# Kernel optimization log

Hardware: AMD Instinct MI355X
Metric: run time of the kernel (lower is better)

## Reference

```python
import jax, jax.numpy as jnp
import numpy as np

N_NODES = 20000
N_EDGES = 320000
DIM = 256
OUT_DIM = 256
N_LAYERS = 2
AVG_LOG = float(np.log(17.0))  # PNA avg_deg['log'] from deg histogram (all degree 16)
STD_EPS = 1e-5
N_AGG = 5
N_SCALER = 3


def _pna_conv(x, edge_index, Wpre, bpre, Wpost, bpost, Wlin, blin):
    """PyG PNAConv (towers=1, pre_layers=1, post_layers=1, divide_input=False)."""
    N = x.shape[0]
    src, dst = edge_index[0], edge_index[1]  # messages flow src -> dst
    # pre_nn on concat([x_i, x_j]) per edge: [E, 2F] -> [E, F]
    m = jnp.concatenate([x[dst], x[src]], axis=-1) @ Wpre.T + bpre
    deg = jax.ops.segment_sum(jnp.ones((src.shape[0],), x.dtype), dst, num_segments=N)
    degc = jnp.maximum(deg, 1.0)[:, None]
    s = jax.ops.segment_sum(m, dst, num_segments=N)
    mean = s / degc
    mean2 = jax.ops.segment_sum(m * m, dst, num_segments=N) / degc
    std = jnp.sqrt(jax.nn.relu(mean2 - mean * mean) + STD_EPS)
    has = (deg > 0)[:, None]
    mn = jnp.where(has, jax.ops.segment_min(m, dst, num_segments=N), 0.0)
    mx = jnp.where(has, jax.ops.segment_max(m, dst, num_segments=N), 0.0)
    agg = jnp.concatenate([mean, s, std, mn, mx], axis=-1)  # [N, 5F]
    logd = jnp.log(degc + 1.0)
    scaled = jnp.concatenate(
        [agg, agg * (logd / AVG_LOG), agg * (AVG_LOG / logd)], axis=-1)  # [N, 15F]
    h = jnp.concatenate([x, scaled], axis=-1) @ Wpost.T + bpost  # [N, F_out]
    return h @ Wlin.T + blin


def setup_inputs() -> dict:
    key = jax.random.key(0)
    ks = jax.random.split(key, 20)
    F = DIM
    L = N_LAYERS
    post_in = (N_AGG * N_SCALER + 1) * F  # 16F = 4096
    sc = 0.05
    inp = {
        "x": jax.random.normal(ks[0], (N_NODES, F), jnp.float32),
        "edge_index_in": jax.random.randint(ks[1], (2, N_EDGES), 0, N_NODES),
        "edge_index_out": jax.random.randint(ks[2], (2, N_EDGES), 0, N_NODES),
    }
    def p(k, shape):
        return sc * jax.random.normal(k, shape, jnp.float32)
    # stacked per-layer params; supply (_s) and demand (_d) channels
    for tag, base in (("s", 3), ("d", 9)):
        inp[f"Wpre_{tag}"] = p(ks[base + 0], (L, F, 2 * F))
        inp[f"bpre_{tag}"] = p(ks[base + 1], (L, F))
        inp[f"Wpost_{tag}"] = p(ks[base + 2], (L, OUT_DIM, post_in))
        inp[f"bpost_{tag}"] = p(ks[base + 3], (L, OUT_DIM))
        inp[f"Wlin_{tag}"] = p(ks[base + 4], (L, OUT_DIM, OUT_DIM))
        inp[f"blin_{tag}"] = p(ks[base + 5], (L, OUT_DIM))
    inp["Wcomb"] = p(ks[15], (L, OUT_DIM, F + 2 * OUT_DIM))
    inp["bcomb"] = p(ks[16], (L, OUT_DIM))
    inp["Wout"] = p(ks[17], (1, OUT_DIM))
    inp["bout"] = p(ks[18], (1,))
    return inp


def reference(x, edge_index_in, edge_index_out,
              Wpre_s, bpre_s, Wpost_s, bpost_s, Wlin_s, blin_s,
              Wpre_d, bpre_d, Wpost_d, bpost_d, Wlin_d, blin_d,
              Wcomb, bcomb, Wout, bout):
    for l in range(N_LAYERS):
        h_in = jax.nn.relu(_pna_conv(x, edge_index_in,
                                     Wpre_s[l], bpre_s[l], Wpost_s[l], bpost_s[l],
                                     Wlin_s[l], blin_s[l]))
        h_out = jax.nn.relu(_pna_conv(x, edge_index_out,
                                      Wpre_d[l], bpre_d[l], Wpost_d[l], bpost_d[l],
                                      Wlin_d[l], blin_d[l]))
        x = jax.nn.relu(jnp.concatenate([x, h_in, h_out], axis=-1) @ Wcomb[l].T + bcomb[l])
    return jnp.squeeze(x @ Wout.T + bout)  # [N]
```

## Files before the change

### kernel.cpp

```cpp
#include <hip/hip_runtime.h>
#include <math.h>

#define NN 20000
#define NE 320000
#define AVG_LOG_F 2.83321334f

typedef unsigned short u16;
typedef _Float16 h8_t __attribute__((ext_vector_type(8)));
typedef float f4_t __attribute__((ext_vector_type(4)));

__device__ __forceinline__ u16 f2h(float f) {
  _Float16 h = (_Float16)f;
  return __builtin_bit_cast(u16, h);
}
__device__ __forceinline__ void gld16(const void* g, void* l) {
  __builtin_amdgcn_global_load_lds(
      (const __attribute__((address_space(1))) void*)g,
      (__attribute__((address_space(3))) void*)l, 16, 0, 0);
}

__global__ __launch_bounds__(256) void k_count2(const int* __restrict__ ein,
                                                const int* __restrict__ eout,
                                                int* __restrict__ deg2, int E) {
  int e = blockIdx.x * 256 + threadIdx.x;
  int ch = blockIdx.y;
  const int* dst = (ch ? eout : ein) + E;
  if (e < E) atomicAdd(&deg2[ch * NN + dst[e]], 1);
}

__global__ __launch_bounds__(1024) void k_scan(const int* __restrict__ deg,
                                               int* __restrict__ rp, int N) {
  __shared__ int lds[1024];
  int t = threadIdx.x;
  int CH = (N + 1023) >> 10;
  int base = t * CH;
  int s = 0;
  for (int i = 0; i < CH; ++i) { int idx = base + i; if (idx < N) s += deg[idx]; }
  lds[t] = s;
  __syncthreads();
  for (int off = 1; off < 1024; off <<= 1) {
    int v = (t >= off) ? lds[t - off] : 0;
    __syncthreads();
    lds[t] += v;
    __syncthreads();
  }
  int run = (t == 0) ? 0 : lds[t - 1];
  for (int i = 0; i < CH; ++i) {
    int idx = base + i;
    if (idx < N) { rp[idx] = run; run += deg[idx]; }
  }
  if (t == 1023) rp[N] = run;
}

__global__ __launch_bounds__(256) void k_scatter2(const int* __restrict__ ein,
                                                  const int* __restrict__ eout,
                                                  const int* __restrict__ rp2,
                                                  int* __restrict__ cur2,
                                                  int* __restrict__ col2, int E) {
  int e = blockIdx.x * 256 + threadIdx.x;
  int ch = blockIdx.y;
  const int* src = (ch ? eout : ein);
  const int* dst = src + E;
  if (e < E) {
    int d = dst[e];
    int p = atomicAdd(&cur2[ch * NN + d], 1);
    col2[rp2[ch * NN + d] + p] = src[e];
  }
}

__global__ __launch_bounds__(256) void k_cvtw(
    const float* __restrict__ Wpre_s, const float* __restrict__ Wpre_d,
    const float* __restrict__ Wlin_s, const float* __restrict__ Wlin_d,
    const float* __restrict__ Wcomb,
    u16* __restrict__ preS, u16* __restrict__ preD,
    u16* __restrict__ lincat, u16* __restrict__ combB) {
  int i = blockIdx.x * 256 + threadIdx.x;
  const float* src;
  u16* dst;
  int so, dofs;
  if (i < 65536)       { src = Wpre_s; dst = preS;  so = i;          dofs = so; }
  else if (i < 131072) { src = Wpre_d; dst = preD;  so = i - 65536;  dofs = so; }
  else if (i < 163840) { int j = i - 131072; int lyr = j >> 14;
                         src = Wlin_s; dst = lincat; so = j; dofs = j + lyr * 16384; }
  else if (i < 196608) { int j = i - 163840; int lyr = j >> 14;
                         src = Wlin_d; dst = lincat; so = j; dofs = j + (lyr + 1) * 16384; }
  else if (i < 294912) { src = Wcomb; dst = combB; so = i - 196608; dofs = so; }
  else return;
  float4 v = *(const float4*)(src + (size_t)so * 4);
  ushort4 o;
  o.x = f2h(v.x); o.y = f2h(v.y); o.z = f2h(v.z); o.w = f2h(v.w);
  *(ushort4*)(dst + (size_t)dofs * 4) = o;
}

__global__ __launch_bounds__(256) void k_cvtx(const float* __restrict__ x,
                                              u16* __restrict__ xc) {
  int i = blockIdx.x * 256 + threadIdx.x;
  int row = i >> 6, c = (i & 63) * 4;
  float4 v = *(const float4*)(x + (size_t)row * 256 + c);
  ushort4 o;
  o.x = f2h(v.x); o.y = f2h(v.y); o.z = f2h(v.z); o.w = f2h(v.w);
  *(ushort4*)(xc + (size_t)row * 768 + c) = o;
}

__global__ __launch_bounds__(256) void k_tc4(const float* __restrict__ Ws,
                                             const float* __restrict__ Wd,
                                             u16* __restrict__ outT) {
  __shared__ float tile[32][33];
  int z = blockIdx.z;
  const float* in = ((z & 1) ? Wd : Ws) + (size_t)(z >> 1) * 256 * 4096;
  u16* out = outT + (size_t)z * (4096 * 256);
  int bx = blockIdx.x, by = blockIdx.y;
  int r = threadIdx.x >> 5, c = threadIdx.x & 31;
#pragma unroll
  for (int it = 0; it < 4; ++it)
    tile[r + it * 8][c] = in[(size_t)(by * 32 + r + it * 8) * 4096 + bx * 32 + c];
  __syncthreads();
#pragma unroll
  for (int it = 0; it < 4; ++it)
    out[(size_t)(bx * 32 + r + it * 8) * 256 + by * 32 + c] = f2h(tile[c][r + it * 8]);
}

__global__ __launch_bounds__(512) void k_mgemm(
    const u16* __restrict__ A, int lda,
    const u16* __restrict__ B, const u16* __restrict__ B2, int ldb, int nsplit,
    const float* __restrict__ bias,
    u16* __restrict__ oH, int ldoH,
    int M, int K, int relu, int zA, int zB, int zO) {
  __shared__ u16 As[2][64 * 64];
  __shared__ u16 Bs[2][256 * 64];
  const int t = threadIdx.x;
  const int z = blockIdx.z;
  A += (size_t)z * zA;
  B += (size_t)z * zB;
  B2 += (size_t)z * zB;
  oH += (size_t)z * zO;
  const int m0 = blockIdx.y * 64;
  const int n0 = blockIdx.x * 256;
  const int l = t & 63, w = t >> 6;
  const int wm = w >> 2, wn = w & 3;
  const int lo = l & 15, hi = l >> 4;

  f4_t acc[2][4];
#pragma unroll
  for (int i = 0; i < 2; ++i)
#pragma unroll
    for (int j = 0; j < 4; ++j) acc[i][j] = (f4_t)0.f;

  const int ra = t >> 3, pa = t & 7;
  const int la = pa ^ (ra & 7);
  int rra = m0 + ra;
  if (rra > M - 1) rra = M - 1;
  const u16* gA = A + (size_t)rra * lda + la * 8;

  const u16* gB[4];
  int lBo[4];
#pragma unroll
  for (int i = 0; i < 4; ++i) {
    int q = i * 512 + t;
    int r = q >> 3, p2 = q & 7;
    int lc = p2 ^ (r & 7);
    int n = n0 + r;
    const u16* bp = (n < nsplit) ? (B + (size_t)n * ldb) : (B2 + (size_t)(n - nsplit) * ldb);
    gB[i] = bp + lc * 8;
    lBo[i] = q * 8;
  }

  gld16(gA, &As[0][t * 8]);
#pragma unroll
  for (int i = 0; i < 4; ++i) gld16(gB[i], &Bs[0][lBo[i]]);
  __syncthreads();

  const int nt = K >> 6;
  for (int tt = 0; tt < nt; ++tt) {
    const int cur = tt & 1;
    if (tt + 1 < nt) {
      const int ko = (tt + 1) << 6;
      gld16(gA + ko, &As[cur ^ 1][t * 8]);
#pragma unroll
      for (int i = 0; i < 4; ++i) gld16(gB[i] + ko, &Bs[cur ^ 1][lBo[i]]);
    }
#pragma unroll
    for (int ks = 0; ks < 2; ++ks) {
      h8_t af[2], bfr[4];
#pragma unroll
      for (int mi = 0; mi < 2; ++mi) {
        int row = wm * 32 + mi * 16 + lo;
        int c = (ks * 4 + hi) ^ (row & 7);
        af[mi] = *(const h8_t*)&As[cur][row * 64 + c * 8];
      }
#pragma unroll
      for (int ni = 0; ni < 4; ++ni) {
        int row = wn * 64 + ni * 16 + lo;
        int c = (ks * 4 + hi) ^ (row & 7);
        bfr[ni] = *(const h8_t*)&Bs[cur][row * 64 + c * 8];
      }
#pragma unroll
      for (int mi = 0; mi < 2; ++mi)
#pragma unroll
        for (int ni = 0; ni < 4; ++ni)
          acc[mi][ni] = __builtin_amdgcn_mfma_f32_16x16x32_f16(
              af[mi], bfr[ni], acc[mi][ni], 0, 0, 0);
    }
    __syncthreads();
  }

  float bv[4];
#pragma unroll
  for (int ni = 0; ni < 4; ++ni) {
    int n = n0 + wn * 64 + ni * 16 + lo;
    bv[ni] = (n < nsplit) ? (bias ? bias[n] : 0.f) : 0.f;
  }
#pragma unroll
  for (int mi = 0; mi < 2; ++mi) {
#pragma unroll
    for (int r = 0; r < 4; ++r) {
      int m = m0 + wm * 32 + mi * 16 + hi * 4 + r;
      if (m < M) {
#pragma unroll
        for (int ni = 0; ni < 4; ++ni) {
          int n = n0 + wn * 64 + ni * 16 + lo;
          float v = acc[mi][ni][r] + bv[ni];
          if (relu && v < 0.f) v = 0.f;
          oH[(size_t)m * ldoH + n] = f2h(v);
        }
      }
    }
  }
}

__global__ __launch_bounds__(512) void k_pgemm(
    const u16* __restrict__ xc, const u16* __restrict__ agg5c,
    const float* __restrict__ scal3c, const u16* __restrict__ Wfl,
    const float* __restrict__ bfl, u16* __restrict__ oHb, int M) {
  __shared__ u16 As[2][64 * 64];
  __shared__ u16 Bs[2][256 * 64];
  const int t = threadIdx.x;
  const int ch = blockIdx.y;
  const u16* agg5 = agg5c + (size_t)ch * NN * 1280;
  const float* scal3 = scal3c + (size_t)ch * NN * 4;
  const u16* Wf = Wfl + (size_t)ch * (256 * 4096);
  const float* bf = bfl + ch * 256;
  u16* oH = oHb + 256 + ch * 256;
  const int m0 = blockIdx.x * 64;
  const int l = t & 63, w = t >> 6;
  const int wm = w >> 2, wn = w & 3;
  const int lo = l & 15, hi = l >> 4;

  f4_t acc[2][4];
#pragma unroll
  for (int i = 0; i < 2; ++i)
#pragma unroll
    for (int j = 0; j < 4; ++j) acc[i][j] = (f4_t)0.f;

  const int ra = t >> 3, pa = t & 7;
  int m = m0 + ra;
  if (m > M - 1) m = M - 1;
  const u16* xrow = xc + (size_t)m * 768;
  const u16* arow = agg5 + (size_t)m * 1280;
  const float s1 = scal3[(size_t)m * 4 + 1];
  const float s2 = scal3[(size_t)m * 4 + 2];
  const int aslot = ra * 64 + (pa ^ (ra & 7)) * 8;

  const u16* gB[4];
  int lBo[4];
#pragma unroll
  for (int i = 0; i < 4; ++i) {
    int q = i * 512 + t;
    int r = q >> 3, p2 = q & 7;
    int lc = p2 ^ (r & 7);
    gB[i] = Wf + (size_t)r * 4096 + lc * 8;
    lBo[i] = q * 8;
  }

  {
    h8_t va = *(const h8_t*)(xrow + pa * 8);
#pragma unroll
    for (int i = 0; i < 4; ++i) gld16(gB[i], &Bs[0][lBo[i]]);
    *(h8_t*)&As[0][aslot] = va;
  }
  __syncthreads();

  for (int tt = 0; tt < 64; ++tt) {
    const int cur = tt & 1;
    h8_t va2 = (h8_t)(_Float16)0.f;
    float fac = 1.f;
    if (tt < 63) {
      int k = ((tt + 1) << 6) + pa * 8;
      const u16* ap;
      if (k < 256) {
        ap = xrow + k;
      } else {
        int q = k - 256;
        int r2 = q < 1280 ? q : (q < 2560 ? q - 1280 : q - 2560);
        fac = q < 1280 ? 1.f : (q < 2560 ? s1 : s2);
        ap = arow + r2;
      }
      va2 = *(const h8_t*)ap;
#pragma unroll
      for (int i = 0; i < 4; ++i) gld16(gB[i] + ((tt + 1) << 6), &Bs[cur ^ 1][lBo[i]]);
    }
#pragma unroll
    for (int ks = 0; ks < 2; ++ks) {
      h8_t af[2], bfr[4];
#pragma unroll
      for (int mi = 0; mi < 2; ++mi) {
        int row = wm * 32 + mi * 16 + lo;
        int c = (ks * 4 + hi) ^ (row & 7);
        af[mi] = *(const h8_t*)&As[cur][row * 64 + c * 8];
      }
#pragma unroll
      for (int ni = 0; ni < 4; ++ni) {
        int row = wn * 64 + ni * 16 + lo;
        int c = (ks * 4 + hi) ^ (row & 7);
        bfr[ni] = *(const h8_t*)&Bs[cur][row * 64 + c * 8];
      }
#pragma unroll
      for (int mi = 0; mi < 2; ++mi)
#pragma unroll
        for (int ni = 0; ni < 4; ++ni)
          acc[mi][ni] = __builtin_amdgcn_mfma_f32_16x16x32_f16(
              af[mi], bfr[ni], acc[mi][ni], 0, 0, 0);
    }
    if (tt < 63) *(h8_t*)&As[cur ^ 1][aslot] = va2 * (_Float16)fac;
    __syncthreads();
  }

  float bv[4];
#pragma unroll
  for (int ni = 0; ni < 4; ++ni) bv[ni] = bf[wn * 64 + ni * 16 + lo];
#pragma unroll
  for (int mi = 0; mi < 2; ++mi) {
#pragma unroll
    for (int r = 0; r < 4; ++r) {
      int mr = m0 + wm * 32 + mi * 16 + hi * 4 + r;
      if (mr < M) {
#pragma unroll
        for (int ni = 0; ni < 4; ++ni) {
          int n = wn * 64 + ni * 16 + lo;
          float vv = acc[mi][ni][r] + bv[ni];
          if (vv < 0.f) vv = 0.f;
          oH[(size_t)mr * 768 + n] = f2h(vv);
        }
      }
    }
  }
}

__global__ __launch_bounds__(256) void k_aggregate(
    const u16* __restrict__ AB, const int* __restrict__ rp,
    const int* __restrict__ col, u16* __restrict__ agg5,
    float* __restrict__ scal3) {
  int w = threadIdx.x >> 6, l = threadIdx.x & 63;
  int n = blockIdx.x * 4 + w;
  int beg = rp[n], end = rp[n + 1];
  int deg = end - beg;
  int half = l >> 5, lf = l & 31;
  float sb[8], qb[8], mnb[8], mxb[8];
#pragma unroll
  for (int j = 0; j < 8; ++j) {
    sb[j] = 0.f; qb[j] = 0.f;
    mnb[j] = 3.402823466e38f; mxb[j] = -3.402823466e38f;
  }
  for (int i = beg + half; i < end; i += 2) {
    int s = col[i];
    h8_t bv = *(const h8_t*)(AB + (size_t)s * 512 + 256 + lf * 8);
#pragma unroll
    for (int j = 0; j < 8; ++j) {
      float b = (float)bv[j];
      sb[j] += b;
      qb[j] = fmaf(b, b, qb[j]);
      mnb[j] = fminf(mnb[j], b);
      mxb[j] = fmaxf(mxb[j], b);
    }
  }
#pragma unroll
  for (int j = 0; j < 8; ++j) {
    sb[j] += __shfl_xor(sb[j], 32, 64);
    qb[j] += __shfl_xor(qb[j], 32, 64);
    mnb[j] = fminf(mnb[j], __shfl_xor(mnb[j], 32, 64));
    mxb[j] = fmaxf(mxb[j], __shfl_xor(mxb[j], 32, 64));
  }
  h8_t cv = *(const h8_t*)(AB + (size_t)n * 512 + lf * 8);
  float degf = (float)deg;
  float degc = degf > 1.f ? degf : 1.f;
  float inv = 1.f / degc;
  float ov[5][8];
#pragma unroll
  for (int j = 0; j < 8; ++j) {
    float c = (float)cv[j];
    float s_m = fmaf(degf, c, sb[j]);
    float mean = s_m * inv;
    float mean2 = fmaf(degf * c, c, fmaf(2.f * c, sb[j], qb[j])) * inv;
    float var = mean2 - mean * mean;
    if (var < 0.f) var = 0.f;
    float sd = sqrtf(var + 1e-5f);
    ov[0][j] = mean;
    ov[1][j] = s_m;
    ov[2][j] = sd;
    ov[3][j] = deg > 0 ? c + mnb[j] : 0.f;
    ov[4][j] = deg > 0 ? c + mxb[j] : 0.f;
  }
  if (half == 0) {
    u16* base = agg5 + (size_t)n * 1280 + lf * 8;
#pragma unroll
    for (int a = 0; a < 5; ++a) {
      h8_t o;
#pragma unroll
      for (int j = 0; j < 8; ++j) o[j] = (_Float16)ov[a][j];
      *(h8_t*)(base + a * 256) = o;
    }
    if (lf == 0) {
      float logd = logf(degc + 1.f);
      float4 sc = make_float4(1.f, logd / AVG_LOG_F, AVG_LOG_F / logd, 0.f);
      *(float4*)(scal3 + (size_t)n * 4) = sc;
    }
  }
}

__global__ __launch_bounds__(256) void k_bfuse4(
    const float* __restrict__ Wlin_s, const float* __restrict__ Wlin_d,
    const float* __restrict__ bpost_s, const float* __restrict__ bpost_d,
    const float* __restrict__ blin_s, const float* __restrict__ blin_d,
    float* __restrict__ bfv4) {
  __shared__ float bp[256];
  int z = blockIdx.x, lyr = z >> 1, ch = z & 1;
  const float* Wlin = (ch ? Wlin_d : Wlin_s) + (size_t)lyr * 65536;
  const float* bpost = (ch ? bpost_d : bpost_s) + lyr * 256;
  const float* blin = (ch ? blin_d : blin_s) + lyr * 256;
  int t = threadIdx.x;
  bp[t] = bpost[t];
  __syncthreads();
  float s = blin[t];
  for (int k = 0; k < 256; ++k) s = fmaf(Wlin[t * 256 + k], bp[k], s);
  bfv4[z * 256 + t] = s;
}

__global__ __launch_bounds__(256) void k_wout(const u16* __restrict__ x,
                                              const float* __restrict__ w,
                                              const float* __restrict__ b,
                                              float* __restrict__ out, int N) {
  int wid = threadIdx.x >> 6, lane = threadIdx.x & 63;
  int n = blockIdx.x * 4 + wid;
  if (n >= N) return;
  ushort4 xv = *(const ushort4*)(x + (size_t)n * 256 + lane * 4);
  const float4 wv = *(const float4*)(w + lane * 4);
  float s = (float)__builtin_bit_cast(_Float16, xv.x) * wv.x +
            (float)__builtin_bit_cast(_Float16, xv.y) * wv.y +
            (float)__builtin_bit_cast(_Float16, xv.z) * wv.z +
            (float)__builtin_bit_cast(_Float16, xv.w) * wv.w;
#pragma unroll
  for (int off = 32; off > 0; off >>= 1) s += __shfl_down(s, off);
  if (lane == 0) out[n] = s + b[0];
}

extern "C" void kernel_launch(void* const* d_in, const int* in_sizes, int n_in,
                              void* d_out, int out_size, void* d_ws, size_t ws_size,
                              hipStream_t stream) {
  const float* x0      = (const float*)d_in[0];
  const int*   ei_in   = (const int*)d_in[1];
  const int*   ei_out  = (const int*)d_in[2];
  const float* Wpre_s  = (const float*)d_in[3];
  const float* bpre_s  = (const float*)d_in[4];
  const float* Wpost_s = (const float*)d_in[5];
  const float* bpost_s = (const float*)d_in[6];
  const float* Wlin_s  = (const float*)d_in[7];
  const float* blin_s  = (const float*)d_in[8];
  const float* Wpre_d  = (const float*)d_in[9];
  const float* bpre_d  = (const float*)d_in[10];
  const float* Wpost_d = (const float*)d_in[11];
  const float* bpost_d = (const float*)d_in[12];
  const float* Wlin_d  = (const float*)d_in[13];
  const float* blin_d  = (const float*)d_in[14];
  const float* Wcomb   = (const float*)d_in[15];
  const float* bcomb   = (const float*)d_in[16];
  const float* Wout    = (const float*)d_in[17];
  const float* bout    = (const float*)d_in[18];
  float* out = (float*)d_out;

  char* p = (char*)d_ws;
  auto alloc = [&](size_t b) {
    char* r = p;
    p += (b + 255) & ~(size_t)255;
    return r;
  };
  int* deg2     = (int*)alloc((size_t)2 * NN * 4);
  int* cur2     = (int*)alloc((size_t)2 * NN * 4);
  int* rp2      = (int*)alloc((size_t)(2 * NN + 1) * 4);
  int* col2     = (int*)alloc((size_t)2 * NE * 4);
  u16* AB       = (u16*)alloc((size_t)NN * 512 * 2);
  u16* agg52    = (u16*)alloc((size_t)2 * NN * 1280 * 2);
  float* scal32 = (float*)alloc((size_t)2 * NN * 4 * 4);
  u16* xcat1    = (u16*)alloc((size_t)NN * 768 * 2);
  u16* xcat2    = (u16*)alloc((size_t)NN * 768 * 2);
  u16* preS     = (u16*)alloc((size_t)2 * 256 * 512 * 2);
  u16* preD     = (u16*)alloc((size_t)2 * 256 * 512 * 2);
  u16* lincat   = (u16*)alloc((size_t)4 * 256 * 256 * 2);
  u16* combB    = (u16*)alloc((size_t)2 * 256 * 768 * 2);
  u16* Wf4      = (u16*)alloc((size_t)4 * 256 * 4096 * 2);
  float* bfv4   = (float*)alloc((size_t)4 * 256 * 4);
  u16* WpostT4  = (u16*)agg52;
  u16* xfin     = xcat1;

  const int BIG = 1 << 30;

  k_cvtw<<<1152, 256, 0, stream>>>(Wpre_s, Wpre_d, Wlin_s, Wlin_d, Wcomb,
                                   preS, preD, lincat, combB);
  k_cvtx<<<5000, 256, 0, stream>>>(x0, xcat1);
  hipMemsetAsync(deg2, 0, (size_t)4 * NN * 4, stream);
  k_count2<<<dim3(1250, 2), 256, 0, stream>>>(ei_in, ei_out, deg2, NE);
  k_scan<<<1, 1024, 0, stream>>>(deg2, rp2, 2 * NN);
  k_scatter2<<<dim3(1250, 2), 256, 0, stream>>>(ei_in, ei_out, rp2, cur2, col2, NE);
  k_tc4<<<dim3(128, 8, 4), 256, 0, stream>>>(Wpost_s, Wpost_d, WpostT4);
  k_mgemm<<<dim3(16, 4, 4), 512, 0, stream>>>(
      lincat, 256, WpostT4, WpostT4, 256, BIG, nullptr,
      Wf4, 4096, 256, 256, 0, 65536, 1048576, 1048576);
  k_bfuse4<<<4, 256, 0, stream>>>(Wlin_s, Wlin_d, bpost_s, bpost_d, blin_s, blin_d, bfv4);

  u16* xcs[2] = {xcat1, xcat2};
  for (int lyr = 0; lyr < 2; ++lyr) {
    u16* xc = xcs[lyr];
    for (int ch = 0; ch < 2; ++ch) {
      u16* preW = ch ? preD : preS;
      const float* bpre = ch ? bpre_d : bpre_s;
      k_mgemm<<<dim3(2, 313, 1), 512, 0, stream>>>(
          xc, 768, preW + (size_t)lyr * 131072, preW + (size_t)lyr * 131072 + 256,
          512, 256, bpre + (size_t)lyr * 256,
          AB, 512, NN, 256, 0, 0, 0, 0);
      k_aggregate<<<5000, 256, 0, stream>>>(
          AB, rp2 + ch * NN, col2,
          agg52 + (size_t)ch * NN * 1280, scal32 + (size_t)ch * NN * 4);
    }
    k_pgemm<<<dim3(313, 2), 512, 0, stream>>>(
        xc, agg52, scal32, Wf4 + (size_t)lyr * 2 * 1048576, bfv4 + lyr * 512, xc, NN);
    if (lyr == 0) {
      k_mgemm<<<dim3(1, 313, 1), 512, 0, stream>>>(
          xc, 768, combB, combB, 768, BIG, bcomb,
          xcat2, 768, NN, 768, 1, 0, 0, 0);
    } else {
      k_mgemm<<<dim3(1, 313, 1), 512, 0, stream>>>(
          xc, 768, combB + 196608, combB + 196608, 768, BIG, bcomb + 256,
          xfin, 256, NN, 768, 1, 0, 0, 0);
    }
  }
  k_wout<<<5000, 256, 0, stream>>>(xfin, Wout, bout, out, NN);
}
```

Baseline: 852.4 us.

## Batch both channels' pre-GEMM and aggregation, single-buffer pgemm LDS

The pre-message GEMM and the aggregation for the supply and demand channels now each run as a single launch over a z/y grid dimension. This uses interleaved pre weights, a per-z bias and a doubled AB buffer, halving launches per layer and giving each kernel more blocks. Separately, k_pgemm's double-buffered LDS pipeline is replaced by a single buffer with load-then-sync per K step. That halves LDS use to allow more resident blocks, but loses the overlap of global loads with MFMA work.

```diff
diff --git a/kernel.cpp b/kernel.cpp
--- a/kernel.cpp
+++ b/kernel.cpp
@@ -72,14 +72,17 @@
     const float* __restrict__ Wpre_s, const float* __restrict__ Wpre_d,
     const float* __restrict__ Wlin_s, const float* __restrict__ Wlin_d,
     const float* __restrict__ Wcomb,
-    u16* __restrict__ preS, u16* __restrict__ preD,
-    u16* __restrict__ lincat, u16* __restrict__ combB) {
+    u16* __restrict__ pre2, u16* __restrict__ lincat, u16* __restrict__ combB) {
   int i = blockIdx.x * 256 + threadIdx.x;
   const float* src;
   u16* dst;
   int so, dofs;
-  if (i < 65536)       { src = Wpre_s; dst = preS;  so = i;          dofs = so; }
-  else if (i < 131072) { src = Wpre_d; dst = preD;  so = i - 65536;  dofs = so; }
+  if (i < 65536)       { int j = i; int lyr = j >> 15;
+                         src = Wpre_s; dst = pre2; so = j;
+                         dofs = (lyr * 2 + 0) * 32768 + (j & 32767); }
+  else if (i < 131072) { int j = i - 65536; int lyr = j >> 15;
+                         src = Wpre_d; dst = pre2; so = j;
+                         dofs = (lyr * 2 + 1) * 32768 + (j & 32767); }
   else if (i < 163840) { int j = i - 131072; int lyr = j >> 14;
                          src = Wlin_s; dst = lincat; so = j; dofs = j + lyr * 16384; }
   else if (i < 196608) { int j = i - 163840; int lyr = j >> 14;
@@ -93,13 +96,21 @@
 }
 
 __global__ __launch_bounds__(256) void k_cvtx(const float* __restrict__ x,
-                                              u16* __restrict__ xc) {
+                                              u16* __restrict__ xc,
+                                              const float* __restrict__ bpre_s,
+                                              const float* __restrict__ bpre_d,
+                                              float* __restrict__ bpre4) {
   int i = blockIdx.x * 256 + threadIdx.x;
   int row = i >> 6, c = (i & 63) * 4;
   float4 v = *(const float4*)(x + (size_t)row * 256 + c);
   ushort4 o;
   o.x = f2h(v.x); o.y = f2h(v.y); o.z = f2h(v.z); o.w = f2h(v.w);
   *(ushort4*)(xc + (size_t)row * 768 + c) = o;
+  if (i < 1024) {
+    int z = i >> 8, n = i & 255;
+    int lyr = z >> 1, ch = z & 1;
+    bpre4[i] = (ch ? bpre_d : bpre_s)[lyr * 256 + n];
+  }
 }
 
 __global__ __launch_bounds__(256) void k_tc4(const float* __restrict__ Ws,
@@ -123,7 +134,7 @@
 __global__ __launch_bounds__(512) void k_mgemm(
     const u16* __restrict__ A, int lda,
     const u16* __restrict__ B, const u16* __restrict__ B2, int ldb, int nsplit,
-    const float* __restrict__ bias,
+    const float* __restrict__ bias, int zBias,
     u16* __restrict__ oH, int ldoH,
     int M, int K, int relu, int zA, int zB, int zO) {
   __shared__ u16 As[2][64 * 64];
@@ -134,6 +145,7 @@
   B += (size_t)z * zB;
   B2 += (size_t)z * zB;
   oH += (size_t)z * zO;
+  if (bias) bias += (size_t)z * zBias;
   const int m0 = blockIdx.y * 64;
   const int n0 = blockIdx.x * 256;
   const int l = t & 63, w = t >> 6;
@@ -232,8 +244,8 @@
     const u16* __restrict__ xc, const u16* __restrict__ agg5c,
     const float* __restrict__ scal3c, const u16* __restrict__ Wfl,
     const float* __restrict__ bfl, u16* __restrict__ oHb, int M) {
-  __shared__ u16 As[2][64 * 64];
-  __shared__ u16 Bs[2][256 * 64];
+  __shared__ u16 As[64 * 64];
+  __shared__ u16 Bs[256 * 64];
   const int t = threadIdx.x;
   const int ch = blockIdx.y;
   const u16* agg5 = agg5c + (size_t)ch * NN * 1280;
@@ -255,50 +267,38 @@
   const int ra = t >> 3, pa = t & 7;
   int m = m0 + ra;
   if (m > M - 1) m = M - 1;
+  u16* ldA = &As[ra * 64 + (pa ^ (ra & 7)) * 8];
   const u16* xrow = xc + (size_t)m * 768;
   const u16* arow = agg5 + (size_t)m * 1280;
-  const float s1 = scal3[(size_t)m * 4 + 1];
-  const float s2 = scal3[(size_t)m * 4 + 2];
-  const int aslot = ra * 64 + (pa ^ (ra & 7)) * 8;
+  const float* srow = scal3 + (size_t)m * 4;
 
   const u16* gB[4];
-  int lBo[4];
+  u16* lB[4];
 #pragma unroll
   for (int i = 0; i < 4; ++i) {
     int q = i * 512 + t;
     int r = q >> 3, p2 = q & 7;
     int lc = p2 ^ (r & 7);
     gB[i] = Wf + (size_t)r * 4096 + lc * 8;
-    lBo[i] = q * 8;
-  }
-
-  {
-    h8_t va = *(const h8_t*)(xrow + pa * 8);
-#pragma unroll
-    for (int i = 0; i < 4; ++i) gld16(gB[i], &Bs[0][lBo[i]]);
-    *(h8_t*)&As[0][aslot] = va;
-  }
-  __syncthreads();
-
-  for (int tt = 0; tt < 64; ++tt) {
-    const int cur = tt & 1;
-    h8_t va2 = (h8_t)(_Float16)0.f;
-    float fac = 1.f;
-    if (tt < 63) {
-      int k = ((tt + 1) << 6) + pa * 8;
-      const u16* ap;
-      if (k < 256) {
-        ap = xrow + k;
-      } else {
-        int q = k - 256;
-        int r2 = q < 1280 ? q : (q < 2560 ? q - 1280 : q - 2560);
-        fac = q < 1280 ? 1.f : (q < 2560 ? s1 : s2);
-        ap = arow + r2;
-      }
-      va2 = *(const h8_t*)ap;
-#pragma unroll
-      for (int i = 0; i < 4; ++i) gld16(gB[i] + ((tt + 1) << 6), &Bs[cur ^ 1][lBo[i]]);
-    }
+    lB[i] = &Bs[q * 8];
+  }
+
+  for (int k0 = 0; k0 < 4096; k0 += 64) {
+#pragma unroll
+    for (int i = 0; i < 4; ++i) gld16(gB[i] + k0, lB[i]);
+    int k = k0 + pa * 8;
+    h8_t v;
+    if (k < 256) {
+      v = *(const h8_t*)(xrow + k);
+    } else {
+      int q = k - 256;
+      int g = q / 1280;
+      int r2 = q - g * 1280;
+      v = *(const h8_t*)(arow + r2);
+      v = v * (_Float16)srow[g];
+    }
+    *(h8_t*)ldA = v;
+    __syncthreads();
 #pragma unroll
     for (int ks = 0; ks < 2; ++ks) {
       h8_t af[2], bfr[4];
@@ -306,13 +306,13 @@
       for (int mi = 0; mi < 2; ++mi) {
         int row = wm * 32 + mi * 16 + lo;
         int c = (ks * 4 + hi) ^ (row & 7);
-        af[mi] = *(const h8_t*)&As[cur][row * 64 + c * 8];
+        af[mi] = *(const h8_t*)&As[row * 64 + c * 8];
       }
 #pragma unroll
       for (int ni = 0; ni < 4; ++ni) {
         int row = wn * 64 + ni * 16 + lo;
         int c = (ks * 4 + hi) ^ (row & 7);
-        bfr[ni] = *(const h8_t*)&Bs[cur][row * 64 + c * 8];
+        bfr[ni] = *(const h8_t*)&Bs[row * 64 + c * 8];
       }
 #pragma unroll
       for (int mi = 0; mi < 2; ++mi)
@@ -321,7 +321,6 @@
           acc[mi][ni] = __builtin_amdgcn_mfma_f32_16x16x32_f16(
               af[mi], bfr[ni], acc[mi][ni], 0, 0, 0);
     }
-    if (tt < 63) *(h8_t*)&As[cur ^ 1][aslot] = va2 * (_Float16)fac;
     __syncthreads();
   }
 
@@ -347,9 +346,14 @@
 }
 
 __global__ __launch_bounds__(256) void k_aggregate(
-    const u16* __restrict__ AB, const int* __restrict__ rp,
-    const int* __restrict__ col, u16* __restrict__ agg5,
-    float* __restrict__ scal3) {
+    const u16* __restrict__ AB2, const int* __restrict__ rp2,
+    const int* __restrict__ col2, u16* __restrict__ agg52,
+    float* __restrict__ scal32) {
+  int ch = blockIdx.y;
+  const u16* AB = AB2 + (size_t)ch * NN * 512;
+  const int* rp = rp2 + ch * NN;
+  u16* agg5 = agg52 + (size_t)ch * NN * 1280;
+  float* scal3 = scal32 + (size_t)ch * NN * 4;
   int w = threadIdx.x >> 6, l = threadIdx.x & 63;
   int n = blockIdx.x * 4 + w;
   int beg = rp[n], end = rp[n + 1];
@@ -362,7 +366,7 @@
     mnb[j] = 3.402823466e38f; mxb[j] = -3.402823466e38f;
   }
   for (int i = beg + half; i < end; i += 2) {
-    int s = col[i];
+    int s = col2[i];
     h8_t bv = *(const h8_t*)(AB + (size_t)s * 512 + 256 + lf * 8);
 #pragma unroll
     for (int j = 0; j < 8; ++j) {
@@ -487,58 +491,52 @@
   int* cur2     = (int*)alloc((size_t)2 * NN * 4);
   int* rp2      = (int*)alloc((size_t)(2 * NN + 1) * 4);
   int* col2     = (int*)alloc((size_t)2 * NE * 4);
-  u16* AB       = (u16*)alloc((size_t)NN * 512 * 2);
+  u16* AB2      = (u16*)alloc((size_t)2 * NN * 512 * 2);
   u16* agg52    = (u16*)alloc((size_t)2 * NN * 1280 * 2);
   float* scal32 = (float*)alloc((size_t)2 * NN * 4 * 4);
   u16* xcat1    = (u16*)alloc((size_t)NN * 768 * 2);
   u16* xcat2    = (u16*)alloc((size_t)NN * 768 * 2);
-  u16* preS     = (u16*)alloc((size_t)2 * 256 * 512 * 2);
-  u16* preD     = (u16*)alloc((size_t)2 * 256 * 512 * 2);
+  u16* pre2     = (u16*)alloc((size_t)4 * 256 * 512 * 2);
   u16* lincat   = (u16*)alloc((size_t)4 * 256 * 256 * 2);
   u16* combB    = (u16*)alloc((size_t)2 * 256 * 768 * 2);
   u16* Wf4      = (u16*)alloc((size_t)4 * 256 * 4096 * 2);
   float* bfv4   = (float*)alloc((size_t)4 * 256 * 4);
+  float* bpre4  = (float*)alloc((size_t)4 * 256 * 4);
   u16* WpostT4  = (u16*)agg52;
   u16* xfin     = xcat1;
 
   const int BIG = 1 << 30;
 
   k_cvtw<<<1152, 256, 0, stream>>>(Wpre_s, Wpre_d, Wlin_s, Wlin_d, Wcomb,
-                                   preS, preD, lincat, combB);
-  k_cvtx<<<5000, 256, 0, stream>>>(x0, xcat1);
+                                   pre2, lincat, combB);
+  k_cvtx<<<5000, 256, 0, stream>>>(x0, xcat1, bpre_s, bpre_d, bpre4);
   hipMemsetAsync(deg2, 0, (size_t)4 * NN * 4, stream);
   k_count2<<<dim3(1250, 2), 256, 0, stream>>>(ei_in, ei_out, deg2, NE);
   k_scan<<<1, 1024, 0, stream>>>(deg2, rp2, 2 * NN);
   k_scatter2<<<dim3(1250, 2), 256, 0, stream>>>(ei_in, ei_out, rp2, cur2, col2, NE);
   k_tc4<<<dim3(128, 8, 4), 256, 0, stream>>>(Wpost_s, Wpost_d, WpostT4);
   k_mgemm<<<dim3(16, 4, 4), 512, 0, stream>>>(
-      lincat, 256, WpostT4, WpostT4, 256, BIG, nullptr,
+      lincat, 256, WpostT4, WpostT4, 256, BIG, nullptr, 0,
       Wf4, 4096, 256, 256, 0, 65536, 1048576, 1048576);
   k_bfuse4<<<4, 256, 0, stream>>>(Wlin_s, Wlin_d, bpost_s, bpost_d, blin_s, blin_d, bfv4);
 
   u16* xcs[2] = {xcat1, xcat2};
   for (int lyr = 0; lyr < 2; ++lyr) {
     u16* xc = xcs[lyr];
-    for (int ch = 0; ch < 2; ++ch) {
-      u16* preW = ch ? preD : preS;
-      const float* bpre = ch ? bpre_d : bpre_s;
-      k_mgemm<<<dim3(2, 313, 1), 512, 0, stream>>>(
-          xc, 768, preW + (size_t)lyr * 131072, preW + (size_t)lyr * 131072 + 256,
-          512, 256, bpre + (size_t)lyr * 256,
-          AB, 512, NN, 256, 0, 0, 0, 0);
-      k_aggregate<<<5000, 256, 0, stream>>>(
-          AB, rp2 + ch * NN, col2,
-          agg52 + (size_t)ch * NN * 1280, scal32 + (size_t)ch * NN * 4);
-    }
+    k_mgemm<<<dim3(2, 313, 2), 512, 0, stream>>>(
+        xc, 768, pre2 + (size_t)lyr * 2 * 131072, pre2 + (size_t)lyr * 2 * 131072 + 256,
+        512, 256, bpre4 + (size_t)lyr * 2 * 256, 256,
+        AB2, 512, NN, 256, 0, 0, 131072, NN * 512);
+    k_aggregate<<<dim3(5000, 2), 256, 0, stream>>>(AB2, rp2, col2, agg52, scal32);
     k_pgemm<<<dim3(313, 2), 512, 0, stream>>>(
         xc, agg52, scal32, Wf4 + (size_t)lyr * 2 * 1048576, bfv4 + lyr * 512, xc, NN);
     if (lyr == 0) {
       k_mgemm<<<dim3(1, 313, 1), 512, 0, stream>>>(
-          xc, 768, combB, combB, 768, BIG, bcomb,
+          xc, 768, combB, combB, 768, BIG, bcomb, 0,
           xcat2, 768, NN, 768, 1, 0, 0, 0);
     } else {
       k_mgemm<<<dim3(1, 313, 1), 512, 0, stream>>>(
-          xc, 768, combB + 196608, combB + 196608, 768, BIG, bcomb + 256,
+          xc, 768, combB + 196608, combB + 196608, 768, BIG, bcomb + 256, 0,
           xfin, 256, NN, 768, 1, 0, 0, 0);
     }
   }
```

Result: faster. 807.9 us (-5.2%).
